# Performance work log

Hardware: AMD Instinct MI355X
Metric: run time of the kernel (lower is better)

The kernel has to match this reference:

```python
import jax, jax.numpy as jnp
import numpy as np


def setup_inputs() -> dict:
    key = jax.random.key(0)
    ks = jax.random.split(key, 32)
    B, S, H, E, Vs, T = 32, 400, 512, 300, 200, 32
    EN, V = 50000, 50200
    rn = lambda k, shape, s=0.05: jax.random.normal(k, shape, jnp.float32) * s
    return {
        'encoder_hidden': rn(ks[0], (B, S, 2 * H), 1.0),
        'hidden0': rn(ks[1], (B, H), 1.0),
        'user_embed': rn(ks[2], (B, E), 1.0),
        'W_embed': rn(ks[3], (EN, E), 1.0),
        'W_ih': rn(ks[4], (3 * H, E)), 'W_hh': rn(ks[5], (3 * H, H)),
        'b_ih': rn(ks[6], (3 * H,)), 'b_hh': rn(ks[7], (3 * H,)),
        'Wk_c': rn(ks[8], (2 * H, H)), 'bk_c': rn(ks[9], (H,)),
        'Wq_c': rn(ks[10], (H, H)), 'bq_c': rn(ks[11], (H,)),
        'we_c': rn(ks[12], (H,)), 'be_c': rn(ks[13], (1,)),
        'Wk_u': rn(ks[14], (E, H)), 'bk_u': rn(ks[15], (H,)),
        'Wq_u': rn(ks[16], (H, H)), 'bq_u': rn(ks[17], (H,)),
        'we_u': rn(ks[18], (H,)), 'be_u': rn(ks[19], (1,)),
        'Wc': rn(ks[20], (3 * H + 2 * E, H)),
        'Wg': rn(ks[21], (3 * H + E,)), 'bg': rn(ks[22], (1,)),
        'Wgen': rn(ks[23], (H, EN)),
        'src_mask': jnp.ones((B, S), jnp.int32),
        'tgt_': jax.random.randint(ks[24], (B, T), 0, EN),
        'specific_vocab': jax.random.randint(ks[25], (B, Vs), 0, EN),
        'vocab_size': V,
    }


def reference(encoder_hidden, hidden0, user_embed, W_embed, W_ih, W_hh, b_ih, b_hh,
              Wk_c, bk_c, Wq_c, bq_c, we_c, be_c, Wk_u, bk_u, Wq_u, bq_u, we_u, be_u,
              Wc, Wg, bg, Wgen, src_mask, tgt_, specific_vocab, vocab_size):
    B, T = tgt_.shape
    # teacher forcing: prev token embed, step 0 uses <s> token id 1
    tgt_embed = W_embed[tgt_]                                  # [B,T,E]
    init_embed = jnp.broadcast_to(W_embed[1], (B, 1, W_embed.shape[1]))
    prev = jnp.concatenate([init_embed, tgt_embed[:, :T - 1]], axis=1)
    xs = jnp.swapaxes(prev, 0, 1)                              # [T,B,E]

    user_vocab_emb = W_embed[specific_vocab]                   # [B,Vs,E]
    proj_key_c = encoder_hidden @ Wk_c + bk_c                  # [B,S,H]
    proj_key_u = user_vocab_emb @ Wk_u + bk_u                  # [B,Vs,H]
    mask = src_mask != 0
    batch_idx = jnp.arange(B)[:, None]

    def gru_cell(h, x):
        gi = x @ W_ih.T + b_ih
        gh = h @ W_hh.T + b_hh
        i_r, i_z, i_n = jnp.split(gi, 3, axis=-1)
        h_r, h_z, h_n = jnp.split(gh, 3, axis=-1)
        r = jax.nn.sigmoid(i_r + h_r)
        z = jax.nn.sigmoid(i_z + h_z)
        n = jnp.tanh(i_n + r * h_n)
        return (1.0 - z) * n + z * h

    def step(h, x):
        h = gru_cell(h, x)                                     # [B,H]
        q = h
        # Bahdanau attention over encoder states
        sc = jnp.tanh((q @ Wq_c + bq_c)[:, None, :] + proj_key_c) @ we_c + be_c  # [B,S]
        sc = jnp.where(mask, sc, -1e9)
        ac = jax.nn.softmax(sc, axis=-1)
        ctx_c = jnp.einsum('bs,bsd->bd', ac, encoder_hidden)   # [B,2H]
        # Bahdanau attention over user-specific vocab embeddings
        su = jnp.tanh((q @ Wq_u + bq_u)[:, None, :] + proj_key_u) @ we_u + be_u  # [B,Vs]
        au = jax.nn.softmax(su, axis=-1)
        ctx_u = jnp.einsum('bv,bve->be', au, user_vocab_emb)   # [B,E]
        ch = jnp.tanh(jnp.concatenate([q, ctx_c, ctx_u, user_embed], axis=-1) @ Wc)
        gen_prob = jax.nn.softmax(ch @ Wgen, axis=-1)          # [B,embed_num]
        gen_prob = jnp.pad(gen_prob, ((0, 0), (0, vocab_size - gen_prob.shape[-1])))
        copy_prob = jnp.zeros((B, vocab_size), gen_prob.dtype).at[batch_idx, specific_vocab].add(au)
        copy_p = jax.nn.sigmoid(jnp.concatenate([ctx_c, q, ctx_u], axis=-1) @ Wg + bg[0])[:, None]
        mix = copy_p * copy_prob + (1.0 - copy_p) * gen_prob   # [B,vocab]
        return h, mix

    _, probs = jax.lax.scan(step, hidden0, xs)                 # [T,B,V]
    return jnp.swapaxes(probs, 0, 1)                           # [B,T,V]
```

## Files before the change

kernel.cpp:

```cpp
#include <hip/hip_runtime.h>


typedef __attribute__((ext_vector_type(8))) short short8;
typedef __attribute__((ext_vector_type(4))) float f32x4;
typedef unsigned short us;

__device__ __forceinline__ float bf2f(us u) {
  return __uint_as_float(((unsigned)u) << 16);
}
__device__ __forceinline__ us f2bf(float f) {
  unsigned x = __float_as_uint(f);
  unsigned r = x + 0x7fffu + ((x >> 16) & 1u);
  return (us)(r >> 16);
}
__device__ __forceinline__ float fsigmoid(float x) { return 1.f / (1.f + __expf(-x)); }
__device__ __forceinline__ float ftanh(float x) {
  float t = __expf(-2.f * fabsf(x));
  float r = (1.f - t) / (1.f + t);
  return x >= 0.f ? r : -r;
}
__device__ __forceinline__ float ftanh_fast(float x) {
  float u = __expf(-2.f * fabsf(x));
  float r = (1.f - u) * __builtin_amdgcn_rcpf(1.f + u);
  return copysignf(r, x);
}


__global__ __launch_bounds__(256) void k_cast_f2b(const float* __restrict__ src,
                                                  us* __restrict__ dst, int n4) {
  int stride = gridDim.x * blockDim.x;
  for (int i = blockIdx.x * blockDim.x + threadIdx.x; i < n4; i += stride) {
    float4 v = ((const float4*)src)[i];
    ushort4 o;
    o.x = f2bf(v.x); o.y = f2bf(v.y); o.z = f2bf(v.z); o.w = f2bf(v.w);
    ((ushort4*)dst)[i] = o;
  }
}

__global__ __launch_bounds__(256) void k_tcastX(const float* __restrict__ src0,
                                                us* __restrict__ dst0,
                                                int R, int C, int Rpad,
                                                size_t srcB, size_t dstB) {
  __shared__ float tile[32][33];
  const float* src = src0 + (size_t)blockIdx.z * srcB;
  us* dst = dst0 + (size_t)blockIdx.z * dstB;
  int c0 = blockIdx.x * 32, r0 = blockIdx.y * 32;
  int tx = threadIdx.x & 31, ty = threadIdx.x >> 5;
#pragma unroll
  for (int i = 0; i < 4; ++i) {
    int r = r0 + ty + i * 8, c = c0 + tx;
    tile[ty + i * 8][tx] = (r < R && c < C) ? src[(size_t)r * C + c] : 0.f;
  }
  __syncthreads();
#pragma unroll
  for (int i = 0; i < 4; ++i) {
    int c = c0 + ty + i * 8, rr = r0 + tx;
    if (c < C && rr < Rpad) dst[(size_t)c * Rpad + rr] = f2bf(tile[tx][ty + i * 8]);
  }
}

__global__ __launch_bounds__(256) void k_tcastXb(const us* __restrict__ src0,
                                                 us* __restrict__ dst0,
                                                 int R, int C, int Rpad,
                                                 size_t srcB, size_t dstB) {
  __shared__ us tile[32][33];
  const us* src = src0 + (size_t)blockIdx.z * srcB;
  us* dst = dst0 + (size_t)blockIdx.z * dstB;
  int c0 = blockIdx.x * 32, r0 = blockIdx.y * 32;
  int tx = threadIdx.x & 31, ty = threadIdx.x >> 5;
#pragma unroll
  for (int i = 0; i < 4; ++i) {
    int r = r0 + ty + i * 8, c = c0 + tx;
    tile[ty + i * 8][tx] = (r < R && c < C) ? src[(size_t)r * C + c] : (us)0;
  }
  __syncthreads();
#pragma unroll
  for (int i = 0; i < 4; ++i) {
    int c = c0 + ty + i * 8, rr = r0 + tx;
    if (c < C && rr < Rpad) dst[(size_t)c * Rpad + rr] = tile[tx][ty + i * 8];
  }
}

__global__ __launch_bounds__(64) void k_castpad(const float* __restrict__ src,
                                                us* __restrict__ dst,
                                                int C, int Cpad) {
  int row = blockIdx.x;
  for (int k = threadIdx.x; k < Cpad; k += 64)
    dst[(size_t)row * Cpad + k] = (k < C) ? f2bf(src[(size_t)row * C + k]) : (us)0;
}

__global__ __launch_bounds__(64) void k_gather_xe(const float* __restrict__ W_embed,
                                                  const int* __restrict__ tgt,
                                                  us* __restrict__ xe) {
  int r = blockIdx.x;
  int t = r >> 5, b = r & 31;
  int tok = (t == 0) ? 1 : tgt[b * 32 + (t - 1)];
  const float* src = W_embed + (size_t)tok * 300;
  for (int k = threadIdx.x; k < 320; k += 64)
    xe[(size_t)r * 320 + k] = (k < 300) ? f2bf(src[k]) : (us)0;
}

__global__ __launch_bounds__(64) void k_gather_uve(const float* __restrict__ W_embed,
                                                   const int* __restrict__ sv,
                                                   us* __restrict__ uve) {
  int row = blockIdx.x;
  int tok = sv[row];
  const float* src = W_embed + (size_t)tok * 300;
  for (int k = threadIdx.x; k < 320; k += 64)
    uve[(size_t)row * 320 + k] = (k < 300) ? f2bf(src[k]) : (us)0;
}

__global__ __launch_bounds__(64) void k_fragpack(const float* __restrict__ W,
                                                 us* __restrict__ F) {
  int q = blockIdx.x, lt = blockIdx.y, kt = blockIdx.z, l = threadIdx.x;
  int localrow = lt * 16 + (l & 15);
  int g = localrow >> 6, jj = localrow & 63;
  const float* src = W + (size_t)(g * 512 + q * 64 + jj) * 512 + kt * 32 + (l >> 4) * 8;
  us* dst = F + (((size_t)(q * 12 + lt) * 16 + kt) * 64 + l) * 8;
#pragma unroll
  for (int i = 0; i < 8; ++i) dst[i] = f2bf(src[i]);
}

template <int MODE>
__global__ __launch_bounds__(512) void gemm_bt(const us* __restrict__ A,
                                               const us* __restrict__ BT,
                                               int M, int N, int K, int Ntiles,
                                               const float* __restrict__ bias,
                                               us* __restrict__ outB,
                                               float* __restrict__ outF,
                                               float* __restrict__ rowsum) {
  __shared__ us As[256 * 32];
  __shared__ us Bs[128 * 32];
  __shared__ float rs[256];
  const int tid = threadIdx.x;
  const int lane = tid & 63, wid = tid >> 6;
  const int wr = wid >> 1, wc = wid & 1;
  const int bx = blockIdx.x;
  const int mt = bx / Ntiles, nt = bx - mt * Ntiles;
  const int m0 = mt * 256, n0 = nt * 128;
  f32x4 acc[4][4] = {};
  for (int kk = 0; kk < K; kk += 32) {
    uint4 av0, av1, bv;
    {
      int c = tid, row = c >> 2, c8 = (c & 3) * 8;
      av0 = *(const uint4*)(A + (size_t)(m0 + row) * K + kk + c8);
      c = tid + 512; row = c >> 2; c8 = (c & 3) * 8;
      av1 = *(const uint4*)(A + (size_t)(m0 + row) * K + kk + c8);
      c = tid; row = c >> 2; c8 = (c & 3) * 8;
      int nr = n0 + row; if (nr > N - 1) nr = N - 1;
      bv = *(const uint4*)(BT + (size_t)nr * K + kk + c8);
    }
    __syncthreads();
    ((uint4*)As)[tid] = av0;
    ((uint4*)As)[tid + 512] = av1;
    ((uint4*)Bs)[tid] = bv;
    __syncthreads();
    short8 af[4], bfr[4];
#pragma unroll
    for (int m = 0; m < 4; ++m)
      af[m] = *(const short8*)(As + (wr * 64 + m * 16 + (lane & 15)) * 32 + (lane >> 4) * 8);
#pragma unroll
    for (int n = 0; n < 4; ++n)
      bfr[n] = *(const short8*)(Bs + (wc * 64 + n * 16 + (lane & 15)) * 32 + (lane >> 4) * 8);
#pragma unroll
    for (int m = 0; m < 4; ++m)
#pragma unroll
      for (int n = 0; n < 4; ++n)
        acc[m][n] = __builtin_amdgcn_mfma_f32_16x16x32_bf16(af[m], bfr[n], acc[m][n], 0, 0, 0);
  }
  if (MODE == 0) {
#pragma unroll
    for (int m = 0; m < 4; ++m)
#pragma unroll
      for (int n = 0; n < 4; ++n)
#pragma unroll
        for (int reg = 0; reg < 4; ++reg) {
          int r = m0 + wr * 64 + m * 16 + (lane >> 4) * 4 + reg;
          int c = n0 + wc * 64 + n * 16 + (lane & 15);
          outB[(size_t)r * N + c] = f2bf(acc[m][n][reg] + bias[c]);
        }
  } else {
    if (tid < 256) rs[tid] = 0.f;
    __syncthreads();
#pragma unroll
    for (int m = 0; m < 4; ++m) {
#pragma unroll
      for (int reg = 0; reg < 4; ++reg) {
        int rloc = wr * 64 + m * 16 + (lane >> 4) * 4 + reg;
        int r = m0 + rloc;
        size_t obase = (size_t)((r & 31) * 32 + (r >> 5)) * 50200;
        float s = 0.f;
#pragma unroll
        for (int n = 0; n < 4; ++n) {
          int c = n0 + wc * 64 + n * 16 + (lane & 15);
          if (c < N) {
            float e = __expf(acc[m][n][reg]);
            if (MODE == 1) outF[obase + c] = e;
            else outB[obase + c] = f2bf(e);
            s += e;
          }
        }
        s += __shfl_xor(s, 1, 64); s += __shfl_xor(s, 2, 64);
        s += __shfl_xor(s, 4, 64); s += __shfl_xor(s, 8, 64);
        if ((lane & 15) == 0) atomicAdd(&rs[rloc], s);
      }
    }
    __syncthreads();
    if (tid < 256) atomicAdd(&rowsum[m0 + tid], rs[tid]);
  }
}

template <int MODE>
__global__ __launch_bounds__(256) void gemm_med(const us* __restrict__ A,
                                                const us* __restrict__ BT,
                                                int M, int N, int K, int Ntiles,
                                                const float* __restrict__ bias,
                                                us* __restrict__ outB) {
  __shared__ us As[64 * 32];
  __shared__ us Bs[128 * 32];
  const int tid = threadIdx.x, lane = tid & 63, w = tid >> 6;
  const int bx = blockIdx.x;
  const int mt = bx / Ntiles, nt = bx - mt * Ntiles;
  const int m0 = mt * 64, n0 = nt * 128;
  f32x4 acc[4][2] = {};
  for (int kk = 0; kk < K; kk += 32) {
    uint4 av, bv0, bv1;
    av = *(const uint4*)(A + (size_t)(m0 + (tid >> 2)) * K + kk + (tid & 3) * 8);
    {
      int i0 = tid * 2, i1 = tid * 2 + 1;
      bv0 = *(const uint4*)(BT + (size_t)(n0 + (i0 >> 2)) * K + kk + (i0 & 3) * 8);
      bv1 = *(const uint4*)(BT + (size_t)(n0 + (i1 >> 2)) * K + kk + (i1 & 3) * 8);
    }
    __syncthreads();
    ((uint4*)As)[tid] = av;
    ((uint4*)Bs)[tid * 2] = bv0;
    ((uint4*)Bs)[tid * 2 + 1] = bv1;
    __syncthreads();
    short8 af[4], bf0, bf1;
#pragma unroll
    for (int m = 0; m < 4; ++m)
      af[m] = *(const short8*)(As + (m * 16 + (lane & 15)) * 32 + (lane >> 4) * 8);
    bf0 = *(const short8*)(Bs + ((w * 2 + 0) * 16 + (lane & 15)) * 32 + (lane >> 4) * 8);
    bf1 = *(const short8*)(Bs + ((w * 2 + 1) * 16 + (lane & 15)) * 32 + (lane >> 4) * 8);
#pragma unroll
    for (int m = 0; m < 4; ++m) {
      acc[m][0] = __builtin_amdgcn_mfma_f32_16x16x32_bf16(af[m], bf0, acc[m][0], 0, 0, 0);
      acc[m][1] = __builtin_amdgcn_mfma_f32_16x16x32_bf16(af[m], bf1, acc[m][1], 0, 0, 0);
    }
  }
#pragma unroll
  for (int m = 0; m < 4; ++m)
#pragma unroll
    for (int q = 0; q < 2; ++q)
#pragma unroll
      for (int reg = 0; reg < 4; ++reg) {
        int r = m0 + m * 16 + (lane >> 4) * 4 + reg;
        int c = n0 + (w * 2 + q) * 16 + (lane & 15);
        float v = acc[m][q][reg];
        if (MODE == 0) v += bias[c];
        else v = ftanh_fast(v);
        outB[(size_t)r * N + c] = f2bf(v);
      }
}

struct GP {
  const us* frag; const us* gib; const float* bhh; const float* hidden0;
  us* hball;
  float* hfall;
  int* arrive;
};

__global__ __launch_bounds__(768, 1) void k_gru(GP P) {
  const int q = blockIdx.x;
  const int tid = threadIdx.x;
  const int lane = tid & 63, w = tid >> 6;
  __shared__ us hs[32 * 512];
  __shared__ float gh[192 * 33];
  short8 bfr[16];
  {
    const us* fb = P.frag + (((size_t)(q * 12 + w) * 16) * 64 + lane) * 8;
#pragma unroll
    for (int kt = 0; kt < 16; ++kt) bfr[kt] = *(const short8*)(fb + (size_t)kt * 512);
  }
  float hprev[3];
#pragma unroll
  for (int s = 0; s < 3; ++s) {
    int i = tid + s * 768;
    if (i < 2048) {
      int b = i >> 6, jj = i & 63;
      hprev[s] = P.hidden0[b * 512 + q * 64 + jj];
    }
  }
  const int sw = (lane & 7) << 3;
  for (int t = 0; t < 32; ++t) {
    if (t > 0) {
      if (tid == 0) {
        while (__hip_atomic_load(P.arrive + (t - 1), __ATOMIC_ACQUIRE,
                                 __HIP_MEMORY_SCOPE_AGENT) < 8) {
          __builtin_amdgcn_s_sleep(1);
        }
      }
      __syncthreads();
    }
    const us* hp = P.hball + (size_t)t * 16384;
    for (int i = tid; i < 2048; i += 768)
      ((uint4*)hs)[i ^ ((i >> 6) & 7)] = *(const uint4*)(hp + i * 8);
    __syncthreads();
    f32x4 acc0 = {}, acc1 = {};
#pragma unroll
    for (int kt = 0; kt < 16; ++kt) {
      int base0 = ((lane & 15) * 512 + kt * 32 + (lane >> 4) * 8) ^ sw;
      int base1 = (((lane & 15) + 16) * 512 + kt * 32 + (lane >> 4) * 8) ^ sw;
      short8 a0 = *(const short8*)(hs + base0);
      short8 a1 = *(const short8*)(hs + base1);
      acc0 = __builtin_amdgcn_mfma_f32_16x16x32_bf16(a0, bfr[kt], acc0, 0, 0, 0);
      acc1 = __builtin_amdgcn_mfma_f32_16x16x32_bf16(a1, bfr[kt], acc1, 0, 0, 0);
    }
    {
      int col = w * 16 + (lane & 15);
#pragma unroll
      for (int reg = 0; reg < 4; ++reg) {
        gh[col * 33 + ((lane >> 4) * 4 + reg)] = acc0[reg];
        gh[col * 33 + (16 + (lane >> 4) * 4 + reg)] = acc1[reg];
      }
    }
    __syncthreads();
    us* hbn = P.hball + (size_t)(t + 1) * 16384;
    float* hfn = P.hfall + (size_t)t * 16384;
#pragma unroll
    for (int s = 0; s < 3; ++s) {
      int i = tid + s * 768;
      if (i < 2048) {
        int b = i >> 6, jj = i & 63;
        int j = q * 64 + jj;
        float g0 = gh[jj * 33 + b] + P.bhh[j];
        float g1 = gh[(64 + jj) * 33 + b] + P.bhh[512 + j];
        float g2 = gh[(128 + jj) * 33 + b] + P.bhh[1024 + j];
        size_t gbase = (size_t)(t * 32 + b) * 1536;
        float r_ = fsigmoid(bf2f(P.gib[gbase + j]) + g0);
        float z_ = fsigmoid(bf2f(P.gib[gbase + 512 + j]) + g1);
        float n_ = ftanh(bf2f(P.gib[gbase + 1024 + j]) + r_ * g2);
        float hv = (1.f - z_) * n_ + z_ * hprev[s];
        hprev[s] = hv;
        hbn[b * 512 + j] = f2bf(hv);
        hfn[b * 512 + j] = hv;
      }
    }
    __syncthreads();
    if (tid == 0)
      __hip_atomic_fetch_add(P.arrive + t, 1, __ATOMIC_RELEASE,
                             __HIP_MEMORY_SCOPE_AGENT);
  }
}

__global__ __launch_bounds__(256) void k_scores(const us* __restrict__ Qall,
                                                const us* __restrict__ pkc,
                                                const us* __restrict__ pku,
                                                const float* __restrict__ wec,
                                                const float* __restrict__ bec,
                                                const float* __restrict__ weu,
                                                const float* __restrict__ beu,
                                                const int* __restrict__ src_mask,
                                                float* __restrict__ sc_enc,
                                                float* __restrict__ sc_usr) {
  __shared__ us q[32 * 512];
  const int bid = blockIdx.x;
  const bool enc = bid < 800;
  int b, s0, qoff, S;
  if (enc) { b = bid / 25; s0 = (bid % 25) * 16; qoff = 0; S = 400; }
  else { int j = bid - 800; b = j / 13; s0 = (j % 13) * 16; qoff = 512; S = 200; }
  for (int i = threadIdx.x; i < 2048; i += 256) {
    int tt = i >> 6, c8 = (i & 63) * 8;
    ((uint4*)q)[i] = *(const uint4*)(Qall + (size_t)(tt * 32 + b) * 1024 + qoff + c8);
  }
  const int w = threadIdx.x >> 6, lane = threadIdx.x & 63;
  const int d0 = lane * 8;
  const float* we = enc ? wec : weu;
  float wef[8];
  {
    float4 w0 = *(const float4*)(we + d0);
    float4 w1 = *(const float4*)(we + d0 + 4);
    wef[0] = w0.x; wef[1] = w0.y; wef[2] = w0.z; wef[3] = w0.w;
    wef[4] = w1.x; wef[5] = w1.y; wef[6] = w1.z; wef[7] = w1.w;
  }
  const float bias = enc ? bec[0] : beu[0];
  float pkf[4][8];
  int ss[4], validv[4], maskedv[4];
#pragma unroll
  for (int si = 0; si < 4; ++si) {
    int s = s0 + w * 4 + si;
    validv[si] = (s < S);
    int sc = validv[si] ? s : (S - 1);
    ss[si] = sc;
    const us* pk = enc ? pkc + ((size_t)b * 400 + sc) * 512
                       : pku + ((size_t)b * 200 + sc) * 512;
    uint4 pkv = *(const uint4*)(pk + d0);
    pkf[si][0] = bf2f((us)(pkv.x & 0xffff)); pkf[si][1] = bf2f((us)(pkv.x >> 16));
    pkf[si][2] = bf2f((us)(pkv.y & 0xffff)); pkf[si][3] = bf2f((us)(pkv.y >> 16));
    pkf[si][4] = bf2f((us)(pkv.z & 0xffff)); pkf[si][5] = bf2f((us)(pkv.z >> 16));
    pkf[si][6] = bf2f((us)(pkv.w & 0xffff)); pkf[si][7] = bf2f((us)(pkv.w >> 16));
    maskedv[si] = enc ? (src_mask[b * 400 + sc] == 0) : 0;
  }
  __syncthreads();
  for (int t = 0; t < 32; ++t) {
    short8 qv = *(const short8*)(q + t * 512 + d0);
    float qf[8];
#pragma unroll
    for (int d = 0; d < 8; ++d) qf[d] = bf2f((us)qv[d]);
#pragma unroll
    for (int si = 0; si < 4; ++si) {
      float a = 0.f;
#pragma unroll
      for (int d = 0; d < 8; ++d) {
        float x = qf[d] + pkf[si][d];
        float u = __expf(-2.f * fabsf(x));
        float r2 = (1.f - u) * __builtin_amdgcn_rcpf(1.f + u);
        a = fmaf(copysignf(r2, x), wef[d], a);
      }
#pragma unroll
      for (int m = 1; m < 64; m <<= 1) a += __shfl_xor(a, m, 64);
      if (lane == 0 && validv[si]) {
        float v = a + bias;
        if (enc) sc_enc[(size_t)(t * 32 + b) * 400 + ss[si]] = maskedv[si] ? -1e9f : v;
        else sc_usr[(size_t)(t * 32 + b) * 200 + ss[si]] = v;
      }
    }
  }
}

__device__ __forceinline__ float bmax256(float v, float* r4, int tid) {
#pragma unroll
  for (int m = 1; m < 64; m <<= 1) v = fmaxf(v, __shfl_xor(v, m, 64));
  if ((tid & 63) == 0) r4[tid >> 6] = v;
  __syncthreads();
  float x = fmaxf(fmaxf(r4[0], r4[1]), fmaxf(r4[2], r4[3]));
  __syncthreads();
  return x;
}
__device__ __forceinline__ float bsum256(float v, float* r4, int tid) {
#pragma unroll
  for (int m = 1; m < 64; m <<= 1) v += __shfl_xor(v, m, 64);
  if ((tid & 63) == 0) r4[tid >> 6] = v;
  __syncthreads();
  float x = r4[0] + r4[1] + r4[2] + r4[3];
  __syncthreads();
  return x;
}

__global__ __launch_bounds__(256) void k_softmax(const float* __restrict__ sc_enc,
                                                 const float* __restrict__ sc_usr,
                                                 const float* __restrict__ bg,
                                                 us* __restrict__ AC,
                                                 us* __restrict__ AU,
                                                 float* __restrict__ aual,
                                                 float* __restrict__ cp_acc) {
  __shared__ float r4[4];
  int r = blockIdx.x, tid = threadIdx.x;
  if (r < 1024) {
    int t = r >> 5, b = r & 31;
    float v0 = (tid < 400) ? sc_enc[(size_t)r * 400 + tid] : -3e38f;
    float v1 = (tid + 256 < 400) ? sc_enc[(size_t)r * 400 + tid + 256] : -3e38f;
    float mx = bmax256(fmaxf(v0, v1), r4, tid);
    float e0 = (tid < 400) ? __expf(v0 - mx) : 0.f;
    float e1 = (tid + 256 < 400) ? __expf(v1 - mx) : 0.f;
    float inv = 1.f / bsum256(e0 + e1, r4, tid);
    us* ACb = AC + (size_t)(b * 32 + t) * 416;
    if (tid < 400) ACb[tid] = f2bf(e0 * inv);
    int s2 = tid + 256;
    if (s2 < 400) ACb[s2] = f2bf(e1 * inv);
    else if (s2 < 416) ACb[s2] = 0;
    if (tid == 0) cp_acc[r] = bg[0];
  } else {
    int rr = r - 1024;
    int t = rr >> 5, b = rr & 31;
    float v0 = (tid < 200) ? sc_usr[(size_t)rr * 200 + tid] : -3e38f;
    float mx = bmax256(v0, r4, tid);
    float e0 = (tid < 200) ? __expf(v0 - mx) : 0.f;
    float inv = 1.f / bsum256(e0, r4, tid);
    us* AUb = AU + (size_t)(b * 32 + t) * 224;
    if (tid < 200) {
      float a = e0 * inv;
      AUb[tid] = f2bf(a);
      aual[(size_t)rr * 200 + tid] = a;
    } else if (tid < 224) {
      AUb[tid] = 0;
    }
  }
}

__global__ __launch_bounds__(256) void k_ctx(const us* __restrict__ A,
                                             const us* __restrict__ BT,
                                             const float* __restrict__ Wg,
                                             us* __restrict__ catall,
                                             float* __restrict__ cp_acc,
                                             int N, int Kp, int catOff, int wgOff,
                                             int Nvalid) {
  __shared__ us As[32 * 32];
  __shared__ us Bs[128 * 32];
  __shared__ float gaccs[32];
  const int b = blockIdx.y, n0 = blockIdx.x * 128;
  const us* Ab = A + (size_t)b * 32 * Kp;
  const us* Bb = BT + (size_t)b * N * Kp;
  const int tid = threadIdx.x, lane = tid & 63, w = tid >> 6;
  if (tid < 32) gaccs[tid] = 0.f;
  f32x4 acc[2][2] = {};
  for (int kk = 0; kk < Kp; kk += 32) {
    uint4 av, bv0, bv1;
    if (tid < 128) av = *(const uint4*)(Ab + (size_t)(tid >> 2) * Kp + kk + (tid & 3) * 8);
    {
      int i0 = tid * 2, row0 = i0 >> 2, c0 = (i0 & 3) * 8;
      int i1 = tid * 2 + 1, row1 = i1 >> 2, c1 = (i1 & 3) * 8;
      int nr0 = n0 + row0; if (nr0 > N - 1) nr0 = N - 1;
      int nr1 = n0 + row1; if (nr1 > N - 1) nr1 = N - 1;
      bv0 = *(const uint4*)(Bb + (size_t)nr0 * Kp + kk + c0);
      bv1 = *(const uint4*)(Bb + (size_t)nr1 * Kp + kk + c1);
    }
    __syncthreads();
    if (tid < 128) ((uint4*)As)[tid] = av;
    ((uint4*)Bs)[tid * 2] = bv0;
    ((uint4*)Bs)[tid * 2 + 1] = bv1;
    __syncthreads();
    short8 a0 = *(const short8*)(As + ((lane & 15)) * 32 + (lane >> 4) * 8);
    short8 a1 = *(const short8*)(As + (16 + (lane & 15)) * 32 + (lane >> 4) * 8);
#pragma unroll
    for (int qq = 0; qq < 2; ++qq) {
      short8 bf_ = *(const short8*)(Bs + ((w * 2 + qq) * 16 + (lane & 15)) * 32 + (lane >> 4) * 8);
      acc[0][qq] = __builtin_amdgcn_mfma_f32_16x16x32_bf16(a0, bf_, acc[0][qq], 0, 0, 0);
      acc[1][qq] = __builtin_amdgcn_mfma_f32_16x16x32_bf16(a1, bf_, acc[1][qq], 0, 0, 0);
    }
  }
#pragma unroll
  for (int mt = 0; mt < 2; ++mt)
#pragma unroll
    for (int qq = 0; qq < 2; ++qq)
#pragma unroll
      for (int reg = 0; reg < 4; ++reg) {
        int t_ = mt * 16 + (lane >> 4) * 4 + reg;
        int c = n0 + (w * 2 + qq) * 16 + (lane & 15);
        if (c < Nvalid) {
          float v = acc[mt][qq][reg];
          catall[(size_t)(t_ * 32 + b) * 2144 + catOff + c] = f2bf(v);
          atomicAdd(&gaccs[t_], v * Wg[wgOff + c]);
        }
      }
  __syncthreads();
  if (tid < 32) atomicAdd(&cp_acc[tid * 32 + b], gaccs[tid]);
}

__global__ __launch_bounds__(256) void k_catgate(const us* __restrict__ hball,
                                                 const float* __restrict__ hfall,
                                                 const float* __restrict__ ue,
                                                 const float* __restrict__ Wg,
                                                 const float* __restrict__ cp_acc,
                                                 us* __restrict__ catall,
                                                 float* __restrict__ cp_all) {
  __shared__ float r4[4];
  int r = blockIdx.x, tid = threadIdx.x;
  int t = r >> 5, b = r & 31;
  us* row = catall + (size_t)r * 2144;
  const us* hb = hball + (size_t)(t + 1) * 16384 + b * 512;
  row[tid] = hb[tid];
  row[256 + tid] = hb[256 + tid];
  float gp = 0.f;
  for (int i = tid; i < 512; i += 256)
    gp += hfall[(size_t)t * 16384 + b * 512 + i] * Wg[1024 + i];
  for (int i = tid; i < 308; i += 256)
    row[1836 + i] = (i < 300) ? f2bf(ue[b * 300 + i]) : (us)0;
  float gtot = bsum256(gp, r4, tid);
  if (tid == 0) cp_all[r] = fsigmoid(gtot + cp_acc[r]);
}

__global__ __launch_bounds__(256) void k_finalize(float* __restrict__ out,
                                                  const float* __restrict__ rowsum,
                                                  const float* __restrict__ cp_all,
                                                  const float* __restrict__ au_all,
                                                  const int* __restrict__ sv) {
  int r = blockIdx.x;
  int t = threadIdx.x;
  int b = r & 31, tt = r >> 5;
  float cp = cp_all[r];
  float scale = (1.f - cp) / rowsum[r];
  float* base = out + (size_t)(b * 32 + tt) * 50200;
  float4* b4 = (float4*)base;
  for (int i = t; i < 12550; i += 256) {
    if (i < 12500) {
      float4 v = b4[i];
      v.x *= scale; v.y *= scale; v.z *= scale; v.w *= scale;
      b4[i] = v;
    } else {
      b4[i] = make_float4(0.f, 0.f, 0.f, 0.f);
    }
  }
  __syncthreads();
  if (t < 200) {
    int idx = sv[b * 200 + t];
    atomicAdd(base + idx, cp * au_all[(size_t)r * 200 + t]);
  }
}

__global__ __launch_bounds__(256) void k_finalize2(const us* __restrict__ expb,
                                                   const float* __restrict__ rowsum,
                                                   const float* __restrict__ cp_all,
                                                   const float* __restrict__ au_all,
                                                   const int* __restrict__ sv,
                                                   float* __restrict__ out) {
  int r = blockIdx.x;
  int t = threadIdx.x;
  int b = r & 31, tt = r >> 5;
  float cp = cp_all[r];
  float scale = (1.f - cp) / rowsum[r];
  size_t obase = (size_t)(b * 32 + tt) * 50200;
  const uint4* eb = (const uint4*)(expb + obase);
  float4* ob = (float4*)(out + obase);
  for (int i = t; i < 6275; i += 256) {
    float4 o0, o1;
    if (i < 6250) {
      uint4 ev = eb[i];
      o0.x = bf2f((us)(ev.x & 0xffff)) * scale; o0.y = bf2f((us)(ev.x >> 16)) * scale;
      o0.z = bf2f((us)(ev.y & 0xffff)) * scale; o0.w = bf2f((us)(ev.y >> 16)) * scale;
      o1.x = bf2f((us)(ev.z & 0xffff)) * scale; o1.y = bf2f((us)(ev.z >> 16)) * scale;
      o1.z = bf2f((us)(ev.w & 0xffff)) * scale; o1.w = bf2f((us)(ev.w >> 16)) * scale;
    } else {
      o0 = make_float4(0.f, 0.f, 0.f, 0.f);
      o1 = o0;
    }
    ob[i * 2] = o0;
    ob[i * 2 + 1] = o1;
  }
  __syncthreads();
  if (t < 200) {
    int idx = sv[b * 200 + t];
    atomicAdd(out + obase + idx, cp * au_all[(size_t)r * 200 + t]);
  }
}


extern "C" void kernel_launch(void* const* d_in, const int* in_sizes, int n_in,
                              void* d_out, int out_size, void* d_ws, size_t ws_size,
                              hipStream_t stream) {
  (void)in_sizes; (void)n_in; (void)out_size;
  const float* enc = (const float*)d_in[0];
  const float* hidden0 = (const float*)d_in[1];
  const float* user_embed = (const float*)d_in[2];
  const float* W_embed = (const float*)d_in[3];
  const float* W_ih = (const float*)d_in[4];
  const float* W_hh = (const float*)d_in[5];
  const float* b_ih = (const float*)d_in[6];
  const float* b_hh = (const float*)d_in[7];
  const float* Wk_c = (const float*)d_in[8];
  const float* bk_c = (const float*)d_in[9];
  const float* Wq_c = (const float*)d_in[10];
  const float* bq_c = (const float*)d_in[11];
  const float* we_c = (const float*)d_in[12];
  const float* be_c = (const float*)d_in[13];
  const float* Wk_u = (const float*)d_in[14];
  const float* bk_u = (const float*)d_in[15];
  const float* Wq_u = (const float*)d_in[16];
  const float* bq_u = (const float*)d_in[17];
  const float* we_u = (const float*)d_in[18];
  const float* be_u = (const float*)d_in[19];
  const float* Wc = (const float*)d_in[20];
  const float* Wg = (const float*)d_in[21];
  const float* bg = (const float*)d_in[22];
  const float* Wgen = (const float*)d_in[23];
  const int* src_mask = (const int*)d_in[24];
  const int* tgt = (const int*)d_in[25];
  const int* sv = (const int*)d_in[26];
  float* out = (float*)d_out;

  char* base = (char*)d_ws;
  size_t off = 0;
  auto take = [&](size_t bytes) {
    char* p = base + off;
    off += (bytes + 255) & ~(size_t)255;
    return p;
  };
  us* WT = (us*)take(50000ull * 512 * 2);
  char* R0 = take(32ull * 1024 * 416 * 2);
  us* encb = (us*)R0;
  us* encTp = (us*)R0;
  char* RCD = take(12800ull * 512 * 2 + 6400ull * 512 * 2);
  us* pkc = (us*)RCD;
  us* pku = (us*)(RCD + 12800ull * 512 * 2);
  us* AC = (us*)RCD;
  us* AU = (us*)(RCD + 860160);
  float* aual = (float*)(RCD + 860160 + 458752);
  us* catall = (us*)(RCD + 860160 + 458752 + 819200);
  us* chb = (us*)(RCD + 860160 + 458752 + 819200 + 4390912);
  char* RU = take(6400ull * 320 * 2);
  us* uve = (us*)RU;
  float* sc_enc = (float*)RU;
  float* sc_usr = (float*)(RU + 1024ull * 400 * 4);
  us* uveTp = (us*)take(32ull * 320 * 224 * 2);
  char* RG = take(2700000);
  us* WkcT = (us*)RG;
  us* WihT = (us*)(RG + 1048576);
  us* xe = (us*)(RG + 1048576 + 983040);
  us* Qall = (us*)RG;
  us* WkuT = (us*)take(512ull * 320 * 2);
  us* WqcuT = (us*)take(1024ull * 512 * 2);
  us* WcT = (us*)take(512ull * 2144 * 2);
  us* WhhF = (us*)take(1536ull * 512 * 2);
  us* gib = (us*)take(1024ull * 1536 * 2);
  us* hball = (us*)take(33ull * 16384 * 2);
  float* hfall = (float*)take(32ull * 16384 * 4);
  float* bqcu = (float*)take(1024 * 4);
  float* cp_acc = (float*)take(1024 * 4);
  float* cp_all = (float*)take(1024 * 4);
  float* rsum = (float*)take(1024 * 4);
  int* arrive = (int*)take(32 * 4);
  size_t expb_bytes = 1024ull * 50200 * 2;
  bool use_bf16exp = (ws_size >= off + expb_bytes + 256);
  us* expb = use_bf16exp ? (us*)take(expb_bytes) : nullptr;

  hipMemcpyAsync(bqcu, bq_c, 512 * 4, hipMemcpyDeviceToDevice, stream);
  hipMemcpyAsync(bqcu + 512, bq_u, 512 * 4, hipMemcpyDeviceToDevice, stream);
  hipMemsetAsync(rsum, 0, 1024 * 4, stream);
  hipMemsetAsync(arrive, 0, 32 * 4, stream);

  k_cast_f2b<<<2048, 256, 0, stream>>>(enc, encb, 3276800);
  k_cast_f2b<<<16, 256, 0, stream>>>(hidden0, hball, 4096);
  k_tcastX<<<dim3(1563, 16, 1), 256, 0, stream>>>(Wgen, WT, 512, 50000, 512, 0, 0);
  k_tcastX<<<dim3(16, 32, 1), 256, 0, stream>>>(Wk_c, WkcT, 1024, 512, 1024, 0, 0);
  k_tcastX<<<dim3(16, 10, 1), 256, 0, stream>>>(Wk_u, WkuT, 300, 512, 320, 0, 0);
  k_tcastX<<<dim3(16, 16, 1), 256, 0, stream>>>(Wq_c, WqcuT, 512, 512, 512, 0, 0);
  k_tcastX<<<dim3(16, 16, 1), 256, 0, stream>>>(Wq_u, WqcuT + 512ull * 512, 512, 512, 512, 0, 0);
  k_tcastX<<<dim3(16, 67, 1), 256, 0, stream>>>(Wc, WcT, 2136, 512, 2144, 0, 0);
  k_castpad<<<1536, 64, 0, stream>>>(W_ih, WihT, 300, 320);
  k_fragpack<<<dim3(8, 12, 16), 64, 0, stream>>>(W_hh, WhhF);
  k_gather_xe<<<1024, 64, 0, stream>>>(W_embed, tgt, xe);
  k_gather_uve<<<6400, 64, 0, stream>>>(W_embed, sv, uve);

  gemm_bt<0><<<200, 512, 0, stream>>>(encb, WkcT, 12800, 512, 1024, 4, bk_c, pkc, nullptr, nullptr);
  gemm_bt<0><<<100, 512, 0, stream>>>(uve, WkuT, 6400, 512, 320, 4, bk_u, pku, nullptr, nullptr);
  gemm_med<0><<<192, 256, 0, stream>>>(xe, WihT, 1024, 1536, 320, 12, b_ih, gib);

  k_tcastX<<<dim3(32, 13, 32), 256, 0, stream>>>(enc, encTp, 400, 1024, 416,
                                                 400ull * 1024, 1024ull * 416);
  k_tcastXb<<<dim3(10, 7, 32), 256, 0, stream>>>(uve, uveTp, 200, 320, 224,
                                                 200ull * 320, 320ull * 224);

  GP gp;
  gp.frag = WhhF; gp.gib = gib; gp.bhh = b_hh; gp.hidden0 = hidden0;
  gp.hball = hball; gp.hfall = hfall; gp.arrive = arrive;
  k_gru<<<8, 768, 0, stream>>>(gp);

  gemm_med<0><<<128, 256, 0, stream>>>(hball + 16384, WqcuT, 1024, 1024, 512, 8,
                                       bqcu, Qall);
  k_scores<<<1216, 256, 0, stream>>>(Qall, pkc, pku, we_c, be_c, we_u, be_u,
                                     src_mask, sc_enc, sc_usr);
  k_softmax<<<2048, 256, 0, stream>>>(sc_enc, sc_usr, bg, AC, AU, aual, cp_acc);
  k_ctx<<<dim3(8, 32), 256, 0, stream>>>(AC, encTp, Wg, catall, cp_acc,
                                         1024, 416, 512, 0, 1024);
  k_ctx<<<dim3(3, 32), 256, 0, stream>>>(AU, uveTp, Wg, catall, cp_acc,
                                         320, 224, 1536, 1536, 300);
  k_catgate<<<1024, 256, 0, stream>>>(hball, hfall, user_embed, Wg, cp_acc,
                                      catall, cp_all);
  gemm_med<2><<<64, 256, 0, stream>>>(catall, WcT, 1024, 512, 2144, 4, nullptr, chb);
  if (use_bf16exp) {
    gemm_bt<3><<<4 * 391, 512, 0, stream>>>(chb, WT, 1024, 50000, 512, 391, nullptr,
                                            expb, nullptr, rsum);
    k_finalize2<<<1024, 256, 0, stream>>>(expb, rsum, cp_all, aual, sv, out);
  } else {
    gemm_bt<1><<<4 * 391, 512, 0, stream>>>(chb, WT, 1024, 50000, 512, 391, nullptr,
                                            nullptr, out, rsum);
    k_finalize<<<1024, 256, 0, stream>>>(out, rsum, cp_all, aual, sv);
  }
}
```

Baseline: 787.6 us.

## Use direct global-to-LDS loads, reorder vocab GEMM tiles, prefetch GRU inputs

The gemm_bt and gemm_med staging loops now use global_load_lds to copy A and B tiles straight into shared memory, with no register round trip. The vocab GEMM walks its blocks M-fastest, so the four row tiles that share a Wgen column tile run close together and can reuse it from L2. In the GRU kernel the gate inputs and b_hh are loaded before the cross-block spin-wait, and every wave's lane 0 now polls the arrival counter, which removes one __syncthreads. tanh is computed with exp2f and a pre-scaled constant. The GRU wait change relies on each wave seeing the flag on its own, which carries memory-ordering risk.

Measured after the change: 870.2 us. 1.1x slower.

```diff
diff --git a/kernel.cpp b/kernel.cpp
--- a/kernel.cpp
+++ b/kernel.cpp
@@ -20,9 +20,14 @@
   return x >= 0.f ? r : -r;
 }
 __device__ __forceinline__ float ftanh_fast(float x) {
-  float u = __expf(-2.f * fabsf(x));
+  float u = exp2f(-2.8853900817779268f * fabsf(x));
   float r = (1.f - u) * __builtin_amdgcn_rcpf(1.f + u);
   return copysignf(r, x);
+}
+__device__ __forceinline__ void gll16(const us* g, us* l) {
+  __builtin_amdgcn_global_load_lds(
+      (const __attribute__((address_space(1))) void*)g,
+      (__attribute__((address_space(3))) void*)l, 16, 0, 0);
 }
 
 
@@ -121,7 +126,7 @@
   for (int i = 0; i < 8; ++i) dst[i] = f2bf(src[i]);
 }
 
-template <int MODE>
+template <int MODE, bool NM = false>
 __global__ __launch_bounds__(512) void gemm_bt(const us* __restrict__ A,
                                                const us* __restrict__ BT,
                                                int M, int N, int K, int Ntiles,
@@ -136,24 +141,18 @@
   const int lane = tid & 63, wid = tid >> 6;
   const int wr = wid >> 1, wc = wid & 1;
   const int bx = blockIdx.x;
-  const int mt = bx / Ntiles, nt = bx - mt * Ntiles;
+  int mt, nt;
+  if (NM) { mt = bx & 3; nt = bx >> 2; }
+  else { mt = bx / Ntiles; nt = bx - mt * Ntiles; }
   const int m0 = mt * 256, n0 = nt * 128;
+  const int arow = tid >> 2, c8 = (tid & 3) * 8;
+  int nr = n0 + arow; if (nr > N - 1) nr = N - 1;
   f32x4 acc[4][4] = {};
   for (int kk = 0; kk < K; kk += 32) {
-    uint4 av0, av1, bv;
-    {
-      int c = tid, row = c >> 2, c8 = (c & 3) * 8;
-      av0 = *(const uint4*)(A + (size_t)(m0 + row) * K + kk + c8);
-      c = tid + 512; row = c >> 2; c8 = (c & 3) * 8;
-      av1 = *(const uint4*)(A + (size_t)(m0 + row) * K + kk + c8);
-      c = tid; row = c >> 2; c8 = (c & 3) * 8;
-      int nr = n0 + row; if (nr > N - 1) nr = N - 1;
-      bv = *(const uint4*)(BT + (size_t)nr * K + kk + c8);
-    }
-    __syncthreads();
-    ((uint4*)As)[tid] = av0;
-    ((uint4*)As)[tid + 512] = av1;
-    ((uint4*)Bs)[tid] = bv;
+    __syncthreads();
+    gll16(A + (size_t)(m0 + arow) * K + kk + c8, As + (size_t)tid * 8);
+    gll16(A + (size_t)(m0 + 128 + arow) * K + kk + c8, As + (size_t)(tid + 512) * 8);
+    gll16(BT + (size_t)nr * K + kk + c8, Bs + (size_t)tid * 8);
     __syncthreads();
     short8 af[4], bfr[4];
 #pragma unroll
@@ -222,19 +221,13 @@
   const int bx = blockIdx.x;
   const int mt = bx / Ntiles, nt = bx - mt * Ntiles;
   const int m0 = mt * 64, n0 = nt * 128;
+  const int row = tid >> 2, c8 = (tid & 3) * 8;
   f32x4 acc[4][2] = {};
   for (int kk = 0; kk < K; kk += 32) {
-    uint4 av, bv0, bv1;
-    av = *(const uint4*)(A + (size_t)(m0 + (tid >> 2)) * K + kk + (tid & 3) * 8);
-    {
-      int i0 = tid * 2, i1 = tid * 2 + 1;
-      bv0 = *(const uint4*)(BT + (size_t)(n0 + (i0 >> 2)) * K + kk + (i0 & 3) * 8);
-      bv1 = *(const uint4*)(BT + (size_t)(n0 + (i1 >> 2)) * K + kk + (i1 & 3) * 8);
-    }
-    __syncthreads();
-    ((uint4*)As)[tid] = av;
-    ((uint4*)Bs)[tid * 2] = bv0;
-    ((uint4*)Bs)[tid * 2 + 1] = bv1;
+    __syncthreads();
+    gll16(A + (size_t)(m0 + row) * K + kk + c8, As + (size_t)tid * 8);
+    gll16(BT + (size_t)(n0 + row) * K + kk + c8, Bs + (size_t)tid * 8);
+    gll16(BT + (size_t)(n0 + 64 + row) * K + kk + c8, Bs + (size_t)(tid + 256) * 8);
     __syncthreads();
     short8 af[4], bf0, bf1;
 #pragma unroll
@@ -282,25 +275,35 @@
 #pragma unroll
     for (int kt = 0; kt < 16; ++kt) bfr[kt] = *(const short8*)(fb + (size_t)kt * 512);
   }
-  float hprev[3];
+  float hprev[3], bh0[3], bh1[3], bh2[3];
 #pragma unroll
   for (int s = 0; s < 3; ++s) {
     int i = tid + s * 768;
     if (i < 2048) {
-      int b = i >> 6, jj = i & 63;
-      hprev[s] = P.hidden0[b * 512 + q * 64 + jj];
+      int b = i >> 6, jj = i & 63, j = q * 64 + jj;
+      hprev[s] = P.hidden0[b * 512 + j];
+      bh0[s] = P.bhh[j]; bh1[s] = P.bhh[512 + j]; bh2[s] = P.bhh[1024 + j];
     }
   }
   const int sw = (lane & 7) << 3;
   for (int t = 0; t < 32; ++t) {
-    if (t > 0) {
-      if (tid == 0) {
-        while (__hip_atomic_load(P.arrive + (t - 1), __ATOMIC_ACQUIRE,
-                                 __HIP_MEMORY_SCOPE_AGENT) < 8) {
-          __builtin_amdgcn_s_sleep(1);
-        }
-      }
-      __syncthreads();
+    float gi0[3], gi1[3], gi2[3];
+#pragma unroll
+    for (int s = 0; s < 3; ++s) {
+      int i = tid + s * 768;
+      if (i < 2048) {
+        int b = i >> 6, jj = i & 63, j = q * 64 + jj;
+        size_t gbase = (size_t)(t * 32 + b) * 1536;
+        gi0[s] = bf2f(P.gib[gbase + j]);
+        gi1[s] = bf2f(P.gib[gbase + 512 + j]);
+        gi2[s] = bf2f(P.gib[gbase + 1024 + j]);
+      }
+    }
+    if (t > 0 && lane == 0) {
+      while (__hip_atomic_load(P.arrive + (t - 1), __ATOMIC_ACQUIRE,
+                               __HIP_MEMORY_SCOPE_AGENT) < 8) {
+        __builtin_amdgcn_s_sleep(1);
+      }
     }
     const us* hp = P.hball + (size_t)t * 16384;
     for (int i = tid; i < 2048; i += 768)
@@ -331,15 +334,13 @@
     for (int s = 0; s < 3; ++s) {
       int i = tid + s * 768;
       if (i < 2048) {
-        int b = i >> 6, jj = i & 63;
-        int j = q * 64 + jj;
-        float g0 = gh[jj * 33 + b] + P.bhh[j];
-        float g1 = gh[(64 + jj) * 33 + b] + P.bhh[512 + j];
-        float g2 = gh[(128 + jj) * 33 + b] + P.bhh[1024 + j];
-        size_t gbase = (size_t)(t * 32 + b) * 1536;
-        float r_ = fsigmoid(bf2f(P.gib[gbase + j]) + g0);
-        float z_ = fsigmoid(bf2f(P.gib[gbase + 512 + j]) + g1);
-        float n_ = ftanh(bf2f(P.gib[gbase + 1024 + j]) + r_ * g2);
+        int b = i >> 6, jj = i & 63, j = q * 64 + jj;
+        float g0 = gh[jj * 33 + b] + bh0[s];
+        float g1 = gh[(64 + jj) * 33 + b] + bh1[s];
+        float g2 = gh[(128 + jj) * 33 + b] + bh2[s];
+        float r_ = fsigmoid(gi0[s] + g0);
+        float z_ = fsigmoid(gi1[s] + g1);
+        float n_ = ftanh(gi2[s] + r_ * g2);
         float hv = (1.f - z_) * n_ + z_ * hprev[s];
         hprev[s] = hv;
         hbn[b * 512 + j] = f2bf(hv);
@@ -413,7 +414,7 @@
 #pragma unroll
       for (int d = 0; d < 8; ++d) {
         float x = qf[d] + pkf[si][d];
-        float u = __expf(-2.f * fabsf(x));
+        float u = exp2f(-2.8853900817779268f * fabsf(x));
         float r2 = (1.f - u) * __builtin_amdgcn_rcpf(1.f + u);
         a = fmaf(copysignf(r2, x), wef[d], a);
       }
@@ -758,12 +759,12 @@
                                       catall, cp_all);
   gemm_med<2><<<64, 256, 0, stream>>>(catall, WcT, 1024, 512, 2144, 4, nullptr, chb);
   if (use_bf16exp) {
-    gemm_bt<3><<<4 * 391, 512, 0, stream>>>(chb, WT, 1024, 50000, 512, 391, nullptr,
-                                            expb, nullptr, rsum);
+    gemm_bt<3, true><<<4 * 391, 512, 0, stream>>>(chb, WT, 1024, 50000, 512, 391,
+                                                  nullptr, expb, nullptr, rsum);
     k_finalize2<<<1024, 256, 0, stream>>>(expb, rsum, cp_all, aual, sv, out);
   } else {
-    gemm_bt<1><<<4 * 391, 512, 0, stream>>>(chb, WT, 1024, 50000, 512, 391, nullptr,
-                                            nullptr, out, rsum);
+    gemm_bt<1, true><<<4 * 391, 512, 0, stream>>>(chb, WT, 1024, 50000, 512, 391,
+                                                  nullptr, nullptr, out, rsum);
     k_finalize<<<1024, 256, 0, stream>>>(out, rsum, cp_all, aual, sv);
   }
 }
```
